# Kernel tuning notes

Measured on AMD Instinct MI355X. Metric: run time of the kernel, lower is better.

Reference implementation:

```python
import jax, jax.numpy as jnp
import numpy as np

B, C, F, T = 8, 2, 1024, 1024
NB, BW, EMB = 64, 16, 128
FEAT = C * BW * 2  # in_channels * bandwidth * reim = 64
EPS = 1e-5


def setup_inputs() -> dict:
    key = jax.random.key(0)
    k1, k2, k3, k4 = jax.random.split(key, 4)
    bound = 1.0 / np.sqrt(FEAT)
    return {
        "x_real": jax.random.normal(k1, (B, C, F, T), dtype=jnp.float32),
        "x_imag": jax.random.normal(k2, (B, C, F, T), dtype=jnp.float32),
        "ln_w": jnp.ones((NB, FEAT), dtype=jnp.float32),
        "ln_b": jnp.zeros((NB, FEAT), dtype=jnp.float32),
        "fc_w": jax.random.uniform(k3, (NB, FEAT, EMB), dtype=jnp.float32, minval=-bound, maxval=bound),
        "fc_b": jax.random.uniform(k4, (NB, EMB), dtype=jnp.float32, minval=-bound, maxval=bound),
    }


def reference(x_real, x_imag, ln_w, ln_b, fc_w, fc_b):
    b, c, f, t = x_real.shape
    nb, feat = ln_w.shape
    bw = f // nb
    # permute (B,C,F,T) -> (B,T,C,F), split F into (nb, bw)
    xr = jnp.transpose(x_real, (0, 3, 1, 2)).reshape(b, t, c, nb, bw)
    xi = jnp.transpose(x_imag, (0, 3, 1, 2)).reshape(b, t, c, nb, bw)
    # view_as_real ordering: feature axis is (C, bw, reim)
    xb = jnp.stack([xr, xi], axis=-1)                 # (B,T,C,nb,bw,2)
    xb = jnp.transpose(xb, (0, 3, 1, 2, 4, 5))        # (B,nb,T,C,bw,2)
    xb = xb.reshape(b, nb, t, feat)                   # (B,nb,T,feat)
    # per-band LayerNorm over last axis
    mean = jnp.mean(xb, axis=-1, keepdims=True)
    var = jnp.mean(jnp.square(xb - mean), axis=-1, keepdims=True)
    xn = (xb - mean) * jax.lax.rsqrt(var + EPS)
    xn = xn * ln_w[None, :, None, :] + ln_b[None, :, None, :]
    # per-band Linear: grouped GEMM over bands
    z = jnp.einsum('bntf,nfe->bnte', xn, fc_w) + fc_b[None, :, None, :]
    return z  # (B, n_bands, T, emb_dim)
```

## Files before the change

kernel.cpp:

```cpp
#include <hip/hip_runtime.h>

#define Bdim   8
#define Cdim   2
#define Fdim   1024
#define Tdim   1024
#define NB     64
#define BWb    16
#define EMB    128
#define FEAT   64
#define TILE_T 64
#define NTHR   256
#define EPSV   1e-5f

typedef __attribute__((ext_vector_type(8))) short bf16x8;
typedef __attribute__((ext_vector_type(4))) float f32x4;

__device__ __forceinline__ unsigned short f2bf(float x) {
    union { float f; unsigned u; } v; v.f = x;
    const unsigned r = v.u + 0x7FFFu + ((v.u >> 16) & 1u);
    return (unsigned short)(r >> 16);
}
__device__ __forceinline__ float bf2f(unsigned short b) {
    union { float f; unsigned u; } v; v.u = ((unsigned)b) << 16;
    return v.f;
}

__global__ __launch_bounds__(256) void conv_w_kernel(
    const float* __restrict__ fcw, unsigned char* __restrict__ ws)
{
    const int n  = blockIdx.x;
    const int e  = threadIdx.x & 127;
    const int fh = (threadIdx.x >> 7) * 32;
    const float* wsrc = fcw + (size_t)n * FEAT * EMB + e;
    float wv[32];
#pragma unroll
    for (int i = 0; i < 32; ++i)
        wv[i] = wsrc[(size_t)(fh + i) * EMB];

    char* const whb = (char*)ws + (size_t)n * 32768 + e * 128;
    char* const wlb = whb + 16384;
#pragma unroll
    for (int cc = 0; cc < 4; ++cc) {
        unsigned hw[4], lw[4];
#pragma unroll
        for (int j = 0; j < 4; ++j) {
            const float x0 = wv[cc * 8 + 2 * j];
            const float x1 = wv[cc * 8 + 2 * j + 1];
            const unsigned short h0 = f2bf(x0), h1 = f2bf(x1);
            hw[j] = (unsigned)h0 | ((unsigned)h1 << 16);
            lw[j] = (unsigned)f2bf(x0 - bf2f(h0))
                  | ((unsigned)f2bf(x1 - bf2f(h1)) << 16);
        }
        const int cs = ((fh >> 3) + cc) ^ (e & 7);
        *(uint4*)(whb + cs * 16) = make_uint4(hw[0], hw[1], hw[2], hw[3]);
        *(uint4*)(wlb + cs * 16) = make_uint4(lw[0], lw[1], lw[2], lw[3]);
    }
}

__global__ __launch_bounds__(NTHR, 3) void bandsplit_mfma(
    const float* __restrict__ xr, const float* __restrict__ xi,
    const float* __restrict__ lnw, const float* __restrict__ lnb,
    const unsigned char* __restrict__ whl, const float* __restrict__ fcb,
    float* __restrict__ out)
{
    __shared__ __align__(16) float xs[FEAT][TILE_T];
    __shared__ __align__(16) unsigned short w_hl[2][EMB][FEAT];
    __shared__ float sb[EMB];
    __shared__ float slnw[FEAT];
    __shared__ float slnb[FEAT];
    __shared__ float smu[TILE_T];
    __shared__ float srs[TILE_T];

    const int tid  = threadIdx.x;
    const int lane = tid & 63;
    const int wav  = tid >> 6;
    const int bid  = blockIdx.x;
    const int tb   = bid & 15;
    const int n    = (bid >> 4) & 63;
    const int b    = bid >> 10;
    const int t0g  = tb * TILE_T;

#pragma unroll
    for (int k = 0; k < 4; ++k) {
        const int v  = tid + k * NTHR;
        const int f  = v >> 4;
        const int tq = v & 15;
        const int c  = f >> 5;
        const int w  = (f >> 1) & 15;
        const float* src = ((f & 1) ? xi : xr)
            + (((size_t)(b * Cdim + c) * Fdim + (n * BWb + w)) * Tdim + t0g + tq * 4);
        *(float4*)&xs[f][tq * 4] = *(const float4*)src;
    }

    if (tid < EMB)            sb[tid]              = fcb[n * EMB + tid];
    else if (tid < EMB + 64)  slnw[tid - EMB]      = lnw[n * FEAT + (tid - EMB)];
    else if (tid < EMB + 128) slnb[tid - EMB - 64] = lnb[n * FEAT + (tid - EMB - 64)];

    {
        const uint4* wsrc = (const uint4*)(whl + (size_t)n * 32768);
        uint4* wdst = (uint4*)&w_hl[0][0][0];
#pragma unroll
        for (int k = 0; k < 8; ++k)
            wdst[tid + k * NTHR] = wsrc[tid + k * NTHR];
    }
    __syncthreads();

    {
        const int t = tid >> 2;
        const int p = tid & 3;
        float s = 0.f, ss = 0.f;
#pragma unroll
        for (int j = 0; j < 16; ++j) {
            const float v = xs[p * 16 + j][t];
            s += v; ss += v * v;
        }
        s += __shfl_xor(s, 1); ss += __shfl_xor(ss, 1);
        s += __shfl_xor(s, 2); ss += __shfl_xor(ss, 2);
        if (p == 0) {
            const float mu  = s * (1.f / 64.f);
            const float var = ss * (1.f / 64.f) - mu * mu;
            smu[t] = mu;
            srs[t] = rsqrtf(var + EPSV);
        }
    }
    __syncthreads();

    uint4 hq[2], lq[2];
    {
        const int t = lane;
        const float mu = smu[t], rsv = srs[t];
#pragma unroll
        for (int u = 0; u < 2; ++u) {
            const int fc = wav + u * 4;
            float xv[8];
#pragma unroll
            for (int j = 0; j < 8; ++j) xv[j] = xs[fc * 8 + j][t];
            unsigned hw[4], lw[4];
#pragma unroll
            for (int j = 0; j < 4; ++j) {
                const int f0 = fc * 8 + 2 * j;
                const float xn0 = (xv[2 * j]     - mu) * rsv * slnw[f0]     + slnb[f0];
                const float xn1 = (xv[2 * j + 1] - mu) * rsv * slnw[f0 + 1] + slnb[f0 + 1];
                const unsigned short h0 = f2bf(xn0), h1 = f2bf(xn1);
                hw[j] = (unsigned)h0 | ((unsigned)h1 << 16);
                lw[j] = (unsigned)f2bf(xn0 - bf2f(h0))
                      | ((unsigned)f2bf(xn1 - bf2f(h1)) << 16);
            }
            hq[u] = make_uint4(hw[0], hw[1], hw[2], hw[3]);
            lq[u] = make_uint4(lw[0], lw[1], lw[2], lw[3]);
        }
    }
    __syncthreads();

    {
        char* const ab = (char*)&xs[0][0];
        const int t = lane;
#pragma unroll
        for (int u = 0; u < 2; ++u) {
            const int fc = wav + u * 4;
            const int cs = fc ^ (t & 7);
            *(uint4*)(ab +        t * 128 + cs * 16) = hq[u];
            *(uint4*)(ab + 8192 + t * 128 + cs * 16) = lq[u];
        }
    }
    __syncthreads();

    const int lr   = lane & 15;
    const int lh   = lane >> 4;
    const int trow = wav * 16;

    f32x4 acc[8];
    const f32x4 zero = {0.f, 0.f, 0.f, 0.f};
#pragma unroll
    for (int et = 0; et < 8; ++et) acc[et] = zero;

    const char* const ab  = (const char*)&xs[0][0];
    const char* const whb = (const char*)&w_hl[0][0][0];
    const char* const wlb = whb + 16384;

#pragma unroll
    for (int ks = 0; ks < 2; ++ks) {
        const int ta = trow + lr;
        const int ca = (ks * 4 + lh) ^ (ta & 7);
        const bf16x8 ahf = *(const bf16x8*)(ab +        ta * 128 + ca * 16);
        const bf16x8 alf = *(const bf16x8*)(ab + 8192 + ta * 128 + ca * 16);
#pragma unroll
        for (int et = 0; et < 8; ++et) {
            const int er = et * 16 + lr;
            const int cw = (ks * 4 + lh) ^ (er & 7);
            const bf16x8 whf = *(const bf16x8*)(whb + er * 128 + cw * 16);
            const bf16x8 wlf = *(const bf16x8*)(wlb + er * 128 + cw * 16);
            acc[et] = __builtin_amdgcn_mfma_f32_16x16x32_bf16(ahf, whf, acc[et], 0, 0, 0);
            acc[et] = __builtin_amdgcn_mfma_f32_16x16x32_bf16(ahf, wlf, acc[et], 0, 0, 0);
            acc[et] = __builtin_amdgcn_mfma_f32_16x16x32_bf16(alf, whf, acc[et], 0, 0, 0);
        }
    }

    const size_t obase = ((size_t)(b * NB + n) * Tdim + (t0g + trow + lh * 4)) * EMB;
#pragma unroll
    for (int et = 0; et < 8; ++et) {
        const int   ec = et * 16 + lr;
        const float be = sb[ec];
#pragma unroll
        for (int r = 0; r < 4; ++r)
            out[obase + (size_t)r * EMB + ec] = acc[et][r] + be;
    }
}

__global__ __launch_bounds__(NTHR, 3) void bandsplit_fallback(
    const float* __restrict__ xr, const float* __restrict__ xi,
    const float* __restrict__ lnw, const float* __restrict__ lnb,
    const float* __restrict__ fcw, const float* __restrict__ fcb,
    float* __restrict__ out)
{
    __shared__ __align__(16) float xs[FEAT][TILE_T];
    __shared__ __align__(16) unsigned short w_hi[EMB][FEAT];
    __shared__ __align__(16) unsigned short w_lo[EMB][FEAT];
    __shared__ float sb[EMB];
    __shared__ float slnw[FEAT];
    __shared__ float slnb[FEAT];
    __shared__ float smu[TILE_T];
    __shared__ float srs[TILE_T];

    const int tid  = threadIdx.x;
    const int lane = tid & 63;
    const int wav  = tid >> 6;
    const int bid  = blockIdx.x;
    const int tb   = bid & 15;
    const int n    = (bid >> 4) & 63;
    const int b    = bid >> 10;
    const int t0g  = tb * TILE_T;

#pragma unroll
    for (int k = 0; k < 4; ++k) {
        const int v  = tid + k * NTHR;
        const int f  = v >> 4;
        const int tq = v & 15;
        const int c  = f >> 5;
        const int w  = (f >> 1) & 15;
        const float* src = ((f & 1) ? xi : xr)
            + (((size_t)(b * Cdim + c) * Fdim + (n * BWb + w)) * Tdim + t0g + tq * 4);
        *(float4*)&xs[f][tq * 4] = *(const float4*)src;
    }

    if (tid < EMB)            sb[tid]              = fcb[n * EMB + tid];
    else if (tid < EMB + 64)  slnw[tid - EMB]      = lnw[n * FEAT + (tid - EMB)];
    else if (tid < EMB + 128) slnb[tid - EMB - 64] = lnb[n * FEAT + (tid - EMB - 64)];

    {
        const int e  = tid & 127;
        const int fh = (tid >> 7) * 32;
        const float* wsrc = fcw + (size_t)n * FEAT * EMB + e;
        float wv[32];
#pragma unroll
        for (int i = 0; i < 32; ++i)
            wv[i] = wsrc[(size_t)(fh + i) * EMB];
        char* const whb = (char*)&w_hi[0][0] + e * 128;
        char* const wlb = (char*)&w_lo[0][0] + e * 128;
#pragma unroll
        for (int cc = 0; cc < 4; ++cc) {
            unsigned hw[4], lw[4];
#pragma unroll
            for (int j = 0; j < 4; ++j) {
                const float x0 = wv[cc * 8 + 2 * j];
                const float x1 = wv[cc * 8 + 2 * j + 1];
                const unsigned short h0 = f2bf(x0), h1 = f2bf(x1);
                hw[j] = (unsigned)h0 | ((unsigned)h1 << 16);
                lw[j] = (unsigned)f2bf(x0 - bf2f(h0))
                      | ((unsigned)f2bf(x1 - bf2f(h1)) << 16);
            }
            const int cs = ((fh >> 3) + cc) ^ (e & 7);
            *(uint4*)(whb + cs * 16) = make_uint4(hw[0], hw[1], hw[2], hw[3]);
            *(uint4*)(wlb + cs * 16) = make_uint4(lw[0], lw[1], lw[2], lw[3]);
        }
    }
    __syncthreads();

    {
        const int t = tid >> 2;
        const int p = tid & 3;
        float s = 0.f, ss = 0.f;
#pragma unroll
        for (int j = 0; j < 16; ++j) {
            const float v = xs[p * 16 + j][t];
            s += v; ss += v * v;
        }
        s += __shfl_xor(s, 1); ss += __shfl_xor(ss, 1);
        s += __shfl_xor(s, 2); ss += __shfl_xor(ss, 2);
        if (p == 0) {
            const float mu  = s * (1.f / 64.f);
            const float var = ss * (1.f / 64.f) - mu * mu;
            smu[t] = mu;
            srs[t] = rsqrtf(var + EPSV);
        }
    }
    __syncthreads();

    uint4 hq[2], lq[2];
    {
        const int t = lane;
        const float mu = smu[t], rsv = srs[t];
#pragma unroll
        for (int u = 0; u < 2; ++u) {
            const int fc = wav + u * 4;
            float xvv[8];
#pragma unroll
            for (int j = 0; j < 8; ++j) xvv[j] = xs[fc * 8 + j][t];
            unsigned hw[4], lw[4];
#pragma unroll
            for (int j = 0; j < 4; ++j) {
                const int f0 = fc * 8 + 2 * j;
                const float xn0 = (xvv[2 * j]     - mu) * rsv * slnw[f0]     + slnb[f0];
                const float xn1 = (xvv[2 * j + 1] - mu) * rsv * slnw[f0 + 1] + slnb[f0 + 1];
                const unsigned short h0 = f2bf(xn0), h1 = f2bf(xn1);
                hw[j] = (unsigned)h0 | ((unsigned)h1 << 16);
                lw[j] = (unsigned)f2bf(xn0 - bf2f(h0))
                      | ((unsigned)f2bf(xn1 - bf2f(h1)) << 16);
            }
            hq[u] = make_uint4(hw[0], hw[1], hw[2], hw[3]);
            lq[u] = make_uint4(lw[0], lw[1], lw[2], lw[3]);
        }
    }
    __syncthreads();

    {
        char* const ab = (char*)&xs[0][0];
        const int t = lane;
#pragma unroll
        for (int u = 0; u < 2; ++u) {
            const int fc = wav + u * 4;
            const int cs = fc ^ (t & 7);
            *(uint4*)(ab +        t * 128 + cs * 16) = hq[u];
            *(uint4*)(ab + 8192 + t * 128 + cs * 16) = lq[u];
        }
    }
    __syncthreads();

    const int lr   = lane & 15;
    const int lh   = lane >> 4;
    const int trow = wav * 16;

    f32x4 acc[8];
    const f32x4 zero = {0.f, 0.f, 0.f, 0.f};
#pragma unroll
    for (int et = 0; et < 8; ++et) acc[et] = zero;

    const char* const ab  = (const char*)&xs[0][0];
    const char* const whb = (const char*)&w_hi[0][0];
    const char* const wlb = (const char*)&w_lo[0][0];

#pragma unroll
    for (int ks = 0; ks < 2; ++ks) {
        const int ta = trow + lr;
        const int ca = (ks * 4 + lh) ^ (ta & 7);
        const bf16x8 ahf = *(const bf16x8*)(ab +        ta * 128 + ca * 16);
        const bf16x8 alf = *(const bf16x8*)(ab + 8192 + ta * 128 + ca * 16);
#pragma unroll
        for (int et = 0; et < 8; ++et) {
            const int er = et * 16 + lr;
            const int cw = (ks * 4 + lh) ^ (er & 7);
            const bf16x8 whf = *(const bf16x8*)(whb + er * 128 + cw * 16);
            const bf16x8 wlf = *(const bf16x8*)(wlb + er * 128 + cw * 16);
            acc[et] = __builtin_amdgcn_mfma_f32_16x16x32_bf16(ahf, whf, acc[et], 0, 0, 0);
            acc[et] = __builtin_amdgcn_mfma_f32_16x16x32_bf16(ahf, wlf, acc[et], 0, 0, 0);
            acc[et] = __builtin_amdgcn_mfma_f32_16x16x32_bf16(alf, whf, acc[et], 0, 0, 0);
        }
    }

    const size_t obase = ((size_t)(b * NB + n) * Tdim + (t0g + trow + lh * 4)) * EMB;
#pragma unroll
    for (int et = 0; et < 8; ++et) {
        const int   ec = et * 16 + lr;
        const float be = sb[ec];
#pragma unroll
        for (int r = 0; r < 4; ++r)
            out[obase + (size_t)r * EMB + ec] = acc[et][r] + be;
    }
}

extern "C" void kernel_launch(void* const* d_in, const int* in_sizes, int n_in,
                              void* d_out, int out_size, void* d_ws, size_t ws_size,
                              hipStream_t stream) {
    const float* xr  = (const float*)d_in[0];
    const float* xi  = (const float*)d_in[1];
    const float* lnw = (const float*)d_in[2];
    const float* lnb = (const float*)d_in[3];
    const float* fcw = (const float*)d_in[4];
    const float* fcb = (const float*)d_in[5];
    float* out = (float*)d_out;

    const int grid = Bdim * NB * (Tdim / TILE_T);
    const size_t wneed = (size_t)NB * 32768;

    if (d_ws != nullptr && ws_size >= wneed) {
        unsigned char* ws = (unsigned char*)d_ws;
        hipLaunchKernelGGL(conv_w_kernel, dim3(NB), dim3(256), 0, stream, fcw, ws);
        hipLaunchKernelGGL(bandsplit_mfma, dim3(grid), dim3(NTHR), 0, stream,
                           xr, xi, lnw, lnb, ws, fcb, out);
    } else {
        hipLaunchKernelGGL(bandsplit_fallback, dim3(grid), dim3(NTHR), 0, stream,
                           xr, xi, lnw, lnb, fcw, fcb, out);
    }
}
```

Measured before the change: 378.9 us.

## Make MFMA blocks persistent over four time tiles with double-buffered prefetch

Each block now handles four consecutive 64-step time tiles for one (batch, band), so the grid is four times smaller. The band's split bf16 weights are loaded into shared memory once and reused across those tiles. The next tile's input is loaded into registers while the current tile is normalized, then written to a second shared buffer. This cuts repeated weight loads and hides global load latency, at the cost of more shared memory, lower launch bounds occupancy (2 instead of 3) and fewer blocks to spread across the GPU.

```diff
diff --git a/kernel.cpp b/kernel.cpp
--- a/kernel.cpp
+++ b/kernel.cpp
@@ -10,6 +10,7 @@
 #define FEAT   64
 #define TILE_T 64
 #define NTHR   256
+#define NTILE  4
 #define EPSV   1e-5f
 
 typedef __attribute__((ext_vector_type(8))) short bf16x8;
@@ -57,13 +58,13 @@
     }
 }
 
-__global__ __launch_bounds__(NTHR, 3) void bandsplit_mfma(
+__global__ __launch_bounds__(NTHR, 2) void bandsplit_pipe(
     const float* __restrict__ xr, const float* __restrict__ xi,
     const float* __restrict__ lnw, const float* __restrict__ lnb,
     const unsigned char* __restrict__ whl, const float* __restrict__ fcb,
     float* __restrict__ out)
 {
-    __shared__ __align__(16) float xs[FEAT][TILE_T];
+    __shared__ __align__(16) float xs2[2][FEAT][TILE_T];
     __shared__ __align__(16) unsigned short w_hl[2][EMB][FEAT];
     __shared__ float sb[EMB];
     __shared__ float slnw[FEAT];
@@ -75,11 +76,13 @@
     const int lane = tid & 63;
     const int wav  = tid >> 6;
     const int bid  = blockIdx.x;
-    const int tb   = bid & 15;
-    const int n    = (bid >> 4) & 63;
-    const int b    = bid >> 10;
-    const int t0g  = tb * TILE_T;
-
+    const int tg   = bid & 3;
+    const int n    = (bid >> 2) & 63;
+    const int b    = bid >> 8;
+    const int tci  = tg * NTILE;
+
+    const float* psrc[4];
+    int fk[4], tqk[4];
 #pragma unroll
     for (int k = 0; k < 4; ++k) {
         const int v  = tid + k * NTHR;
@@ -87,123 +90,142 @@
         const int tq = v & 15;
         const int c  = f >> 5;
         const int w  = (f >> 1) & 15;
-        const float* src = ((f & 1) ? xi : xr)
-            + (((size_t)(b * Cdim + c) * Fdim + (n * BWb + w)) * Tdim + t0g + tq * 4);
-        *(float4*)&xs[f][tq * 4] = *(const float4*)src;
-    }
-
+        fk[k]  = f;
+        tqk[k] = tq;
+        psrc[k] = ((f & 1) ? xi : xr)
+                + ((size_t)(b * Cdim + c) * Fdim + (n * BWb + w)) * Tdim + tq * 4;
+    }
+
+    {
+        const uint4* wsrc = (const uint4*)(whl + (size_t)n * 32768);
+        uint4* wdst = (uint4*)&w_hl[0][0][0];
+#pragma unroll
+        for (int k = 0; k < 8; ++k)
+            wdst[tid + k * NTHR] = wsrc[tid + k * NTHR];
+    }
     if (tid < EMB)            sb[tid]              = fcb[n * EMB + tid];
     else if (tid < EMB + 64)  slnw[tid - EMB]      = lnw[n * FEAT + (tid - EMB)];
     else if (tid < EMB + 128) slnb[tid - EMB - 64] = lnb[n * FEAT + (tid - EMB - 64)];
-
-    {
-        const uint4* wsrc = (const uint4*)(whl + (size_t)n * 32768);
-        uint4* wdst = (uint4*)&w_hl[0][0][0];
-#pragma unroll
-        for (int k = 0; k < 8; ++k)
-            wdst[tid + k * NTHR] = wsrc[tid + k * NTHR];
-    }
-    __syncthreads();
-
-    {
-        const int t = tid >> 2;
-        const int p = tid & 3;
-        float s = 0.f, ss = 0.f;
-#pragma unroll
-        for (int j = 0; j < 16; ++j) {
-            const float v = xs[p * 16 + j][t];
-            s += v; ss += v * v;
-        }
-        s += __shfl_xor(s, 1); ss += __shfl_xor(ss, 1);
-        s += __shfl_xor(s, 2); ss += __shfl_xor(ss, 2);
-        if (p == 0) {
-            const float mu  = s * (1.f / 64.f);
-            const float var = ss * (1.f / 64.f) - mu * mu;
-            smu[t] = mu;
-            srs[t] = rsqrtf(var + EPSV);
-        }
-    }
-    __syncthreads();
-
-    uint4 hq[2], lq[2];
-    {
-        const int t = lane;
-        const float mu = smu[t], rsv = srs[t];
-#pragma unroll
-        for (int u = 0; u < 2; ++u) {
-            const int fc = wav + u * 4;
-            float xv[8];
-#pragma unroll
-            for (int j = 0; j < 8; ++j) xv[j] = xs[fc * 8 + j][t];
-            unsigned hw[4], lw[4];
-#pragma unroll
-            for (int j = 0; j < 4; ++j) {
-                const int f0 = fc * 8 + 2 * j;
-                const float xn0 = (xv[2 * j]     - mu) * rsv * slnw[f0]     + slnb[f0];
-                const float xn1 = (xv[2 * j + 1] - mu) * rsv * slnw[f0 + 1] + slnb[f0 + 1];
-                const unsigned short h0 = f2bf(xn0), h1 = f2bf(xn1);
-                hw[j] = (unsigned)h0 | ((unsigned)h1 << 16);
-                lw[j] = (unsigned)f2bf(xn0 - bf2f(h0))
-                      | ((unsigned)f2bf(xn1 - bf2f(h1)) << 16);
-            }
-            hq[u] = make_uint4(hw[0], hw[1], hw[2], hw[3]);
-            lq[u] = make_uint4(lw[0], lw[1], lw[2], lw[3]);
-        }
-    }
-    __syncthreads();
-
-    {
-        char* const ab = (char*)&xs[0][0];
-        const int t = lane;
-#pragma unroll
-        for (int u = 0; u < 2; ++u) {
-            const int fc = wav + u * 4;
-            const int cs = fc ^ (t & 7);
-            *(uint4*)(ab +        t * 128 + cs * 16) = hq[u];
-            *(uint4*)(ab + 8192 + t * 128 + cs * 16) = lq[u];
-        }
-    }
+#pragma unroll
+    for (int k = 0; k < 4; ++k)
+        *(float4*)&xs2[0][fk[k]][tqk[k] * 4] = *(const float4*)(psrc[k] + tci * TILE_T);
     __syncthreads();
 
     const int lr   = lane & 15;
     const int lh   = lane >> 4;
     const int trow = wav * 16;
-
-    f32x4 acc[8];
-    const f32x4 zero = {0.f, 0.f, 0.f, 0.f};
-#pragma unroll
-    for (int et = 0; et < 8; ++et) acc[et] = zero;
-
-    const char* const ab  = (const char*)&xs[0][0];
     const char* const whb = (const char*)&w_hl[0][0][0];
     const char* const wlb = whb + 16384;
 
-#pragma unroll
-    for (int ks = 0; ks < 2; ++ks) {
-        const int ta = trow + lr;
-        const int ca = (ks * 4 + lh) ^ (ta & 7);
-        const bf16x8 ahf = *(const bf16x8*)(ab +        ta * 128 + ca * 16);
-        const bf16x8 alf = *(const bf16x8*)(ab + 8192 + ta * 128 + ca * 16);
+    for (int tt = 0; tt < NTILE; ++tt) {
+        const int cur = tt & 1;
+        const int t0g = (tci + tt) * TILE_T;
+        char* const ab = (char*)&xs2[cur][0][0];
+
+        float4 stg[4];
+        if (tt < NTILE - 1) {
+#pragma unroll
+            for (int k = 0; k < 4; ++k)
+                stg[k] = *(const float4*)(psrc[k] + t0g + TILE_T);
+        }
+
+        {
+            const int t = tid >> 2;
+            const int p = tid & 3;
+            float s = 0.f, ss = 0.f;
+#pragma unroll
+            for (int j = 0; j < 16; ++j) {
+                const float v = xs2[cur][p * 16 + j][t];
+                s += v; ss += v * v;
+            }
+            s += __shfl_xor(s, 1); ss += __shfl_xor(ss, 1);
+            s += __shfl_xor(s, 2); ss += __shfl_xor(ss, 2);
+            if (p == 0) {
+                const float mu  = s * (1.f / 64.f);
+                const float var = ss * (1.f / 64.f) - mu * mu;
+                smu[t] = mu;
+                srs[t] = rsqrtf(var + EPSV);
+            }
+        }
+        __syncthreads();
+
+        uint4 hq[2], lq[2];
+        {
+            const int t = lane;
+            const float mu = smu[t], rsv = srs[t];
+#pragma unroll
+            for (int u = 0; u < 2; ++u) {
+                const int fc = wav + u * 4;
+                float xv[8];
+#pragma unroll
+                for (int j = 0; j < 8; ++j) xv[j] = xs2[cur][fc * 8 + j][t];
+                unsigned hw[4], lw[4];
+#pragma unroll
+                for (int j = 0; j < 4; ++j) {
+                    const int f0 = fc * 8 + 2 * j;
+                    const float xn0 = (xv[2 * j]     - mu) * rsv * slnw[f0]     + slnb[f0];
+                    const float xn1 = (xv[2 * j + 1] - mu) * rsv * slnw[f0 + 1] + slnb[f0 + 1];
+                    const unsigned short h0 = f2bf(xn0), h1 = f2bf(xn1);
+                    hw[j] = (unsigned)h0 | ((unsigned)h1 << 16);
+                    lw[j] = (unsigned)f2bf(xn0 - bf2f(h0))
+                          | ((unsigned)f2bf(xn1 - bf2f(h1)) << 16);
+                }
+                hq[u] = make_uint4(hw[0], hw[1], hw[2], hw[3]);
+                lq[u] = make_uint4(lw[0], lw[1], lw[2], lw[3]);
+            }
+        }
+        __syncthreads();
+
+        {
+            const int t = lane;
+#pragma unroll
+            for (int u = 0; u < 2; ++u) {
+                const int fc = wav + u * 4;
+                const int cs = fc ^ (t & 7);
+                *(uint4*)(ab +        t * 128 + cs * 16) = hq[u];
+                *(uint4*)(ab + 8192 + t * 128 + cs * 16) = lq[u];
+            }
+        }
+        if (tt < NTILE - 1) {
+            const int nxt = cur ^ 1;
+#pragma unroll
+            for (int k = 0; k < 4; ++k)
+                *(float4*)&xs2[nxt][fk[k]][tqk[k] * 4] = stg[k];
+        }
+        __syncthreads();
+
+        f32x4 acc[8];
+        const f32x4 zero = {0.f, 0.f, 0.f, 0.f};
+#pragma unroll
+        for (int et = 0; et < 8; ++et) acc[et] = zero;
+
+#pragma unroll
+        for (int ks = 0; ks < 2; ++ks) {
+            const int ta = trow + lr;
+            const int ca = (ks * 4 + lh) ^ (ta & 7);
+            const bf16x8 ahf = *(const bf16x8*)(ab +        ta * 128 + ca * 16);
+            const bf16x8 alf = *(const bf16x8*)(ab + 8192 + ta * 128 + ca * 16);
+#pragma unroll
+            for (int et = 0; et < 8; ++et) {
+                const int er = et * 16 + lr;
+                const int cw = (ks * 4 + lh) ^ (er & 7);
+                const bf16x8 whf = *(const bf16x8*)(whb + er * 128 + cw * 16);
+                const bf16x8 wlf = *(const bf16x8*)(wlb + er * 128 + cw * 16);
+                acc[et] = __builtin_amdgcn_mfma_f32_16x16x32_bf16(ahf, whf, acc[et], 0, 0, 0);
+                acc[et] = __builtin_amdgcn_mfma_f32_16x16x32_bf16(ahf, wlf, acc[et], 0, 0, 0);
+                acc[et] = __builtin_amdgcn_mfma_f32_16x16x32_bf16(alf, whf, acc[et], 0, 0, 0);
+            }
+        }
+
+        const size_t obase = ((size_t)(b * NB + n) * Tdim + (t0g + trow + lh * 4)) * EMB;
 #pragma unroll
         for (int et = 0; et < 8; ++et) {
-            const int er = et * 16 + lr;
-            const int cw = (ks * 4 + lh) ^ (er & 7);
-            const bf16x8 whf = *(const bf16x8*)(whb + er * 128 + cw * 16);
-            const bf16x8 wlf = *(const bf16x8*)(wlb + er * 128 + cw * 16);
-            acc[et] = __builtin_amdgcn_mfma_f32_16x16x32_bf16(ahf, whf, acc[et], 0, 0, 0);
-            acc[et] = __builtin_amdgcn_mfma_f32_16x16x32_bf16(ahf, wlf, acc[et], 0, 0, 0);
-            acc[et] = __builtin_amdgcn_mfma_f32_16x16x32_bf16(alf, whf, acc[et], 0, 0, 0);
-        }
-    }
-
-    const size_t obase = ((size_t)(b * NB + n) * Tdim + (t0g + trow + lh * 4)) * EMB;
-#pragma unroll
-    for (int et = 0; et < 8; ++et) {
-        const int   ec = et * 16 + lr;
-        const float be = sb[ec];
-#pragma unroll
-        for (int r = 0; r < 4; ++r)
-            out[obase + (size_t)r * EMB + ec] = acc[et][r] + be;
+            const int   ec = et * 16 + lr;
+            const float be = sb[ec];
+#pragma unroll
+            for (int r = 0; r < 4; ++r)
+                out[obase + (size_t)r * EMB + ec] = acc[et][r] + be;
+        }
     }
 }
 
@@ -389,15 +411,16 @@
     const float* fcb = (const float*)d_in[5];
     float* out = (float*)d_out;
 
-    const int grid = Bdim * NB * (Tdim / TILE_T);
     const size_t wneed = (size_t)NB * 32768;
 
     if (d_ws != nullptr && ws_size >= wneed) {
         unsigned char* ws = (unsigned char*)d_ws;
+        const int grid = Bdim * NB * (Tdim / (TILE_T * NTILE));
         hipLaunchKernelGGL(conv_w_kernel, dim3(NB), dim3(256), 0, stream, fcw, ws);
-        hipLaunchKernelGGL(bandsplit_mfma, dim3(grid), dim3(NTHR), 0, stream,
+        hipLaunchKernelGGL(bandsplit_pipe, dim3(grid), dim3(NTHR), 0, stream,
                            xr, xi, lnw, lnb, ws, fcb, out);
     } else {
+        const int grid = Bdim * NB * (Tdim / TILE_T);
         hipLaunchKernelGGL(bandsplit_fallback, dim3(grid), dim3(NTHR), 0, stream,
                            xr, xi, lnw, lnb, fcw, fcb, out);
     }
```

Result: slower. 392.0 us (+3.5%).

## Repartition MFMA work so each wave owns an embedding slice with register-cached weights

Applied to the files above, without the earlier changes.

Each wave previously computed 16 time rows across all 128 embedding columns, reading weight fragments from LDS for every MFMA. Now each wave owns 32 embedding columns across all 64 time rows. It preloads its weight fragments (hi and lo bf16 split) into registers once, before the LayerNorm phase, and streams activation fragments from LDS instead. This cuts LDS reads of weights and overlaps them with the normalization work, at the cost of more live registers and more activation reads per wave.

```diff
diff --git a/kernel.cpp b/kernel.cpp
--- a/kernel.cpp
+++ b/kernel.cpp
@@ -105,6 +105,23 @@
     }
     __syncthreads();
 
+    const int lr = lane & 15;
+    const int lh = lane >> 4;
+    const char* const whb = (const char*)&w_hl[0][0][0];
+    const char* const wlb = whb + 16384;
+
+    bf16x8 wf_h[2][2], wf_l[2][2];
+#pragma unroll
+    for (int et2 = 0; et2 < 2; ++et2) {
+        const int er = wav * 32 + et2 * 16 + lr;
+#pragma unroll
+        for (int ks = 0; ks < 2; ++ks) {
+            const int cw = (ks * 4 + lh) ^ (er & 7);
+            wf_h[et2][ks] = *(const bf16x8*)(whb + er * 128 + cw * 16);
+            wf_l[et2][ks] = *(const bf16x8*)(wlb + er * 128 + cw * 16);
+        }
+    }
+
     {
         const int t = tid >> 2;
         const int p = tid & 3;
@@ -165,45 +182,44 @@
     }
     __syncthreads();
 
-    const int lr   = lane & 15;
-    const int lh   = lane >> 4;
-    const int trow = wav * 16;
-
-    f32x4 acc[8];
+    const char* const ab = (const char*)&xs[0][0];
+
+    f32x4 acc[4][2];
     const f32x4 zero = {0.f, 0.f, 0.f, 0.f};
 #pragma unroll
-    for (int et = 0; et < 8; ++et) acc[et] = zero;
-
-    const char* const ab  = (const char*)&xs[0][0];
-    const char* const whb = (const char*)&w_hl[0][0][0];
-    const char* const wlb = whb + 16384;
-
-#pragma unroll
-    for (int ks = 0; ks < 2; ++ks) {
-        const int ta = trow + lr;
-        const int ca = (ks * 4 + lh) ^ (ta & 7);
-        const bf16x8 ahf = *(const bf16x8*)(ab +        ta * 128 + ca * 16);
-        const bf16x8 alf = *(const bf16x8*)(ab + 8192 + ta * 128 + ca * 16);
-#pragma unroll
-        for (int et = 0; et < 8; ++et) {
-            const int er = et * 16 + lr;
-            const int cw = (ks * 4 + lh) ^ (er & 7);
-            const bf16x8 whf = *(const bf16x8*)(whb + er * 128 + cw * 16);
-            const bf16x8 wlf = *(const bf16x8*)(wlb + er * 128 + cw * 16);
-            acc[et] = __builtin_amdgcn_mfma_f32_16x16x32_bf16(ahf, whf, acc[et], 0, 0, 0);
-            acc[et] = __builtin_amdgcn_mfma_f32_16x16x32_bf16(ahf, wlf, acc[et], 0, 0, 0);
-            acc[et] = __builtin_amdgcn_mfma_f32_16x16x32_bf16(alf, whf, acc[et], 0, 0, 0);
-        }
-    }
-
-    const size_t obase = ((size_t)(b * NB + n) * Tdim + (t0g + trow + lh * 4)) * EMB;
-#pragma unroll
-    for (int et = 0; et < 8; ++et) {
-        const int   ec = et * 16 + lr;
-        const float be = sb[ec];
-#pragma unroll
-        for (int r = 0; r < 4; ++r)
-            out[obase + (size_t)r * EMB + ec] = acc[et][r] + be;
+    for (int tg = 0; tg < 4; ++tg)
+#pragma unroll
+        for (int et2 = 0; et2 < 2; ++et2) acc[tg][et2] = zero;
+
+#pragma unroll
+    for (int tg = 0; tg < 4; ++tg) {
+        const int ta = tg * 16 + lr;
+#pragma unroll
+        for (int ks = 0; ks < 2; ++ks) {
+            const int ca = (ks * 4 + lh) ^ (ta & 7);
+            const bf16x8 ahf = *(const bf16x8*)(ab +        ta * 128 + ca * 16);
+            const bf16x8 alf = *(const bf16x8*)(ab + 8192 + ta * 128 + ca * 16);
+#pragma unroll
+            for (int et2 = 0; et2 < 2; ++et2) {
+                acc[tg][et2] = __builtin_amdgcn_mfma_f32_16x16x32_bf16(ahf, wf_h[et2][ks], acc[tg][et2], 0, 0, 0);
+                acc[tg][et2] = __builtin_amdgcn_mfma_f32_16x16x32_bf16(ahf, wf_l[et2][ks], acc[tg][et2], 0, 0, 0);
+                acc[tg][et2] = __builtin_amdgcn_mfma_f32_16x16x32_bf16(alf, wf_h[et2][ks], acc[tg][et2], 0, 0, 0);
+            }
+        }
+    }
+
+    const size_t orow0 = (size_t)(b * NB + n) * Tdim + t0g;
+#pragma unroll
+    for (int tg = 0; tg < 4; ++tg) {
+        const size_t obase = (orow0 + tg * 16 + lh * 4) * EMB;
+#pragma unroll
+        for (int et2 = 0; et2 < 2; ++et2) {
+            const int   ec = wav * 32 + et2 * 16 + lr;
+            const float be = sb[ec];
+#pragma unroll
+            for (int r = 0; r < 4; ++r)
+                out[obase + (size_t)r * EMB + ec] = acc[tg][et2][r] + be;
+        }
     }
 }
 
```

Measured after the change: 374.4 us. Within noise of the previous version (-1.2%).
